# Kernel tuning notes

Hardware: AMD Instinct MI355X
Metric: run time of the kernel (lower is better)

## Reference

```python
import jax, jax.numpy as jnp
import numpy as np

B, I, H = 512, 2048, 2048


def setup_inputs() -> dict:
    key = jax.random.key(0)
    ks = jax.random.split(key, 14)
    s = 0.02  # weight init scale
    inp = {
        "inputs": jax.random.normal(ks[0], (B, I), jnp.float32),
        "states": jax.random.normal(ks[1], (2, B, H), jnp.float32),
        "Wi": jax.random.normal(ks[2], (I, H), jnp.float32) * s,
        "Ui": jax.random.normal(ks[3], (H, H), jnp.float32) * s,
        "bi": jnp.zeros((H,), jnp.float32),
        "Wf": jax.random.normal(ks[4], (I, H), jnp.float32) * s,
        "Uf": jax.random.normal(ks[5], (H, H), jnp.float32) * s,
        "bf": jnp.zeros((H,), jnp.float32),
        "Wg": jax.random.normal(ks[6], (I, H), jnp.float32) * s,
        "Ug": jax.random.normal(ks[7], (H, H), jnp.float32) * s,
        "bg": jnp.zeros((H,), jnp.float32),
        "Wc": jax.random.normal(ks[8], (I, H), jnp.float32) * s,
        "Uc": jax.random.normal(ks[9], (H, H), jnp.float32) * s,
        "bc": jnp.zeros((H,), jnp.float32),
    }
    return inp


def reference(inputs, states, Wi, Ui, bi, Wf, Uf, bf, Wg, Ug, bg, Wc, Uc, bc):
    # Faithful to the original cell, including its quirks:
    # recurrent matmuls use states[0] (prevstate); c mixes states[1] (prevoutput).
    prevstate, prevoutput = states[0], states[1]  # [B,H] each
    i = jax.nn.sigmoid(inputs @ Wi + prevstate @ Ui + bi)
    f = jax.nn.sigmoid(inputs @ Wf + prevstate @ Uf + bf)
    g = jax.nn.sigmoid(inputs @ Wg + prevstate @ Ug + bg)
    c_ = jnp.tanh(inputs @ Wc + prevstate @ Uc + bc)
    c = f * prevoutput + i * c_
    state = g * jnp.tanh(c)
    return c, jnp.stack([state, c])
```

## Files before the change

### kernel.cpp

```cpp
#include <hip/hip_runtime.h>

#define BH (512*2048)
#define PPLANE (512ull*8192ull)
#define PLANE_BYTES (PPLANE*2ull)

typedef __attribute__((ext_vector_type(8))) short short8;
typedef __attribute__((ext_vector_type(4))) float floatx4;
typedef __attribute__((ext_vector_type(4))) unsigned int uint4v;
typedef __attribute__((ext_vector_type(8))) unsigned short ushort8v;

__device__ inline unsigned pk2(float a, float b){
    unsigned ua = __builtin_bit_cast(unsigned, a) + 0x8000u;
    unsigned ub = __builtin_bit_cast(unsigned, b) + 0x8000u;
    return __builtin_amdgcn_perm(ub, ua, 0x07060302u);
}
__device__ inline unsigned short f2bf1(float x){
    return (unsigned short)((__builtin_bit_cast(unsigned, x) + 0x8000u) >> 16);
}
__device__ inline float bf2f(unsigned short s){
    return __builtin_bit_cast(float, ((unsigned)s) << 16);
}
__device__ inline int swz(int r, int g){ return r*4 + (g ^ ((r>>1)&3)); }

__device__ inline float fsig(float x){ return __builtin_amdgcn_rcpf(1.f + __expf(-x)); }
__device__ inline float ftanh(float x){ return 2.f*fsig(2.f*x) - 1.f; }

__global__ __launch_bounds__(256, 2) void gemm_tile(
    const float* __restrict__ inputs, const float* __restrict__ states,
    const float* __restrict__ Wi, const float* __restrict__ Ui,
    const float* __restrict__ Wf, const float* __restrict__ Uf,
    const float* __restrict__ Wg, const float* __restrict__ Ug,
    const float* __restrict__ Wc, const float* __restrict__ Uc,
    unsigned short* __restrict__ P, int KB)
{
    __shared__ uint4v As[2][512];
    __shared__ uint4v Bs[2][512];

    const int t    = threadIdx.x;
    const int m0   = blockIdx.y * 128;
    const int z    = blockIdx.z;
    const int nblk = blockIdx.x;
    const int gate = nblk >> 4;
    const int c0   = (nblk & 15) * 128;
    const int gk   = z * KB;

    const float* Abase; const float* Bsel; int ko;
    if (gk < 2048) {
        Abase = inputs; ko = gk;
        switch (gate){ case 0: Bsel=Wi; break; case 1: Bsel=Wf; break;
                       case 2: Bsel=Wg; break; default: Bsel=Wc; }
    } else {
        Abase = states; ko = gk - 2048;
        switch (gate){ case 0: Bsel=Ui; break; case 1: Bsel=Uf; break;
                       case 2: Bsel=Ug; break; default: Bsel=Uc; }
    }
    const int NIT = KB >> 5;

    const int lane  = t & 63;
    const int wave  = t >> 6;
    const int wm    = (wave & 1) * 64;
    const int wn    = (wave >> 1) * 64;
    const int row16 = lane & 15;
    const int g4    = lane >> 4;

    const int ar  = t >> 2;
    const int ag  = t & 3;
    const int bn  = t & 127;
    const int bg2 = (t >> 7) * 2;

    const float* Ap = Abase + (size_t)(m0 + ar) * 2048 + ko + ag * 8;
    const float* Bp = Bsel  + (size_t)ko * 2048 + c0 + bn;

    floatx4 acc[4][4];
    #pragma unroll
    for (int i = 0; i < 4; i++)
        #pragma unroll
        for (int j = 0; j < 4; j++)
            acc[i][j] = (floatx4){0.f,0.f,0.f,0.f};

    floatx4 a0,a1,a2,a3;
    float b0[8], b1[8];

    a0 = *(const floatx4*)Ap;            a1 = *(const floatx4*)(Ap + 4);
    a2 = *(const floatx4*)(Ap + 64*2048); a3 = *(const floatx4*)(Ap + 64*2048 + 4);
    #pragma unroll
    for (int j = 0; j < 8; j++) b0[j] = Bp[(size_t)(bg2*8 + j) * 2048];
    #pragma unroll
    for (int j = 0; j < 8; j++) b1[j] = Bp[(size_t)(bg2*8 + 8 + j) * 2048];
    {
        uint4v w;
        w.x=pk2(a0[0],a0[1]); w.y=pk2(a0[2],a0[3]); w.z=pk2(a1[0],a1[1]); w.w=pk2(a1[2],a1[3]);
        As[0][swz(ar, ag)] = w;
        w.x=pk2(a2[0],a2[1]); w.y=pk2(a2[2],a2[3]); w.z=pk2(a3[0],a3[1]); w.w=pk2(a3[2],a3[3]);
        As[0][swz(ar+64, ag)] = w;
        w.x=pk2(b0[0],b0[1]); w.y=pk2(b0[2],b0[3]); w.z=pk2(b0[4],b0[5]); w.w=pk2(b0[6],b0[7]);
        Bs[0][swz(bn, bg2)] = w;
        w.x=pk2(b1[0],b1[1]); w.y=pk2(b1[2],b1[3]); w.z=pk2(b1[4],b1[5]); w.w=pk2(b1[6],b1[7]);
        Bs[0][swz(bn, bg2+1)] = w;
    }

    for (int kk = 0; kk < NIT; kk++) {
        __syncthreads();
        const int cur = kk & 1;

        if (kk + 1 < NIT) {
            const float* ap = Ap + (kk+1) * 32;
            a0 = *(const floatx4*)ap;             a1 = *(const floatx4*)(ap + 4);
            a2 = *(const floatx4*)(ap + 64*2048); a3 = *(const floatx4*)(ap + 64*2048 + 4);
            const float* bp = Bp + (size_t)(kk+1) * 32 * 2048;
            #pragma unroll
            for (int j = 0; j < 8; j++) b0[j] = bp[(size_t)(bg2*8 + j) * 2048];
            #pragma unroll
            for (int j = 0; j < 8; j++) b1[j] = bp[(size_t)(bg2*8 + 8 + j) * 2048];
        }

        short8 afr[4], bfr[4];
        #pragma unroll
        for (int mi = 0; mi < 4; mi++)
            afr[mi] = *(const short8*)&As[cur][swz(wm + mi*16 + row16, g4)];
        #pragma unroll
        for (int ni = 0; ni < 4; ni++)
            bfr[ni] = *(const short8*)&Bs[cur][swz(wn + ni*16 + row16, g4)];
        #pragma unroll
        for (int mi = 0; mi < 4; mi++)
            #pragma unroll
            for (int ni = 0; ni < 4; ni++)
                acc[mi][ni] = __builtin_amdgcn_mfma_f32_16x16x32_bf16(
                    afr[mi], bfr[ni], acc[mi][ni], 0, 0, 0);

        if (kk + 1 < NIT) {
            const int nxt = cur ^ 1;
            uint4v w;
            w.x=pk2(a0[0],a0[1]); w.y=pk2(a0[2],a0[3]); w.z=pk2(a1[0],a1[1]); w.w=pk2(a1[2],a1[3]);
            As[nxt][swz(ar, ag)] = w;
            w.x=pk2(a2[0],a2[1]); w.y=pk2(a2[2],a2[3]); w.z=pk2(a3[0],a3[1]); w.w=pk2(a3[2],a3[3]);
            As[nxt][swz(ar+64, ag)] = w;
            w.x=pk2(b0[0],b0[1]); w.y=pk2(b0[2],b0[3]); w.z=pk2(b0[4],b0[5]); w.w=pk2(b0[6],b0[7]);
            Bs[nxt][swz(bn, bg2)] = w;
            w.x=pk2(b1[0],b1[1]); w.y=pk2(b1[2],b1[3]); w.z=pk2(b1[4],b1[5]); w.w=pk2(b1[6],b1[7]);
            Bs[nxt][swz(bn, bg2+1)] = w;
        }
    }

    unsigned short* dst = P + (size_t)z * PPLANE;
    const int gbase = gate * 2048 + c0;
    #pragma unroll
    for (int mi = 0; mi < 4; mi++)
        #pragma unroll
        for (int ni = 0; ni < 4; ni++)
            #pragma unroll
            for (int j = 0; j < 4; j++) {
                int row = m0 + wm + mi*16 + g4*4 + j;
                int col = gbase + wn + ni*16 + row16;
                dst[(size_t)row * 8192 + col] = f2bf1(acc[mi][ni][j]);
            }
}

__global__ __launch_bounds__(256) void combine_kernel(
    float* __restrict__ out, const unsigned short* __restrict__ P,
    const float* __restrict__ states,
    const float* __restrict__ bi, const float* __restrict__ bfv,
    const float* __restrict__ bg, const float* __restrict__ bc, int nz)
{
    const int idx = (blockIdx.x * 256 + threadIdx.x) * 8;
    const int row = idx >> 11;
    const int h   = idx & 2047;
    const size_t base = (size_t)row * 8192 + h;

    float xi[8], xf[8], xg[8], xc[8];
    #pragma unroll
    for (int e = 0; e < 8; e++) {
        xi[e] = bi[h+e]; xf[e] = bfv[h+e]; xg[e] = bg[h+e]; xc[e] = bc[h+e];
    }
    for (int z = 0; z < nz; z++) {
        const unsigned short* Pz = P + (size_t)z * PPLANE;
        ushort8v vi = *(const ushort8v*)&Pz[base];
        ushort8v vf = *(const ushort8v*)&Pz[base + 2048];
        ushort8v vg = *(const ushort8v*)&Pz[base + 4096];
        ushort8v vc = *(const ushort8v*)&Pz[base + 6144];
        #pragma unroll
        for (int e = 0; e < 8; e++) {
            xi[e] += bf2f(vi[e]); xf[e] += bf2f(vf[e]);
            xg[e] += bf2f(vg[e]); xc[e] += bf2f(vc[e]);
        }
    }

    const float* po = states + BH;
    floatx4 pov[2];
    pov[0] = *(const floatx4*)&po[idx];
    pov[1] = *(const floatx4*)&po[idx + 4];

    floatx4 vcv[2], vsv[2];
    #pragma unroll
    for (int q = 0; q < 2; q++)
        #pragma unroll
        for (int j = 0; j < 4; j++) {
            int e = q*4 + j;
            float c = fsig(xf[e]) * pov[q][j] + fsig(xi[e]) * ftanh(xc[e]);
            vcv[q][j] = c;
            vsv[q][j] = fsig(xg[e]) * ftanh(c);
        }
    #pragma unroll
    for (int q = 0; q < 2; q++) {
        *(floatx4*)&out[idx + q*4]          = vcv[q];
        *(floatx4*)&out[BH + idx + q*4]     = vsv[q];
        *(floatx4*)&out[2*BH + idx + q*4]   = vcv[q];
    }
}

extern "C" void kernel_launch(void* const* d_in, const int* in_sizes, int n_in,
                              void* d_out, int out_size, void* d_ws, size_t ws_size,
                              hipStream_t stream) {
    const float* inputs = (const float*)d_in[0];
    const float* states = (const float*)d_in[1];
    const float* Wi = (const float*)d_in[2];
    const float* Ui = (const float*)d_in[3];
    const float* bi = (const float*)d_in[4];
    const float* Wf = (const float*)d_in[5];
    const float* Uf = (const float*)d_in[6];
    const float* bf = (const float*)d_in[7];
    const float* Wg = (const float*)d_in[8];
    const float* Ug = (const float*)d_in[9];
    const float* bg = (const float*)d_in[10];
    const float* Wc = (const float*)d_in[11];
    const float* Uc = (const float*)d_in[12];
    const float* bc = (const float*)d_in[13];
    float* out = (float*)d_out;
    unsigned short* P = (unsigned short*)d_ws;

    const int nz = (ws_size >= 4 * PLANE_BYTES) ? 4 : 2;
    const int KB = 4096 / nz;

    dim3 grid(64, 4, nz);
    gemm_tile<<<grid, 256, 0, stream>>>(inputs, states, Wi, Ui, Wf, Uf,
                                        Wg, Ug, Wc, Uc, P, KB);
    combine_kernel<<<BH / (8 * 256), 256, 0, stream>>>(out, P, states,
                                                       bi, bf, bg, bc, nz);
}
```

Measured before the change: 238.1 us.

## Deepen global-load prefetch to two stages with ping-pong register sets

Restructures the GEMM main loop to keep two register sets (X/Y) of global loads in flight, issuing loads two K-steps ahead instead of one, and unrolls the loop by two. This aims to hide global memory latency for the fp32 A/B tiles better before they are converted to bf16 and stored to LDS. It roughly doubles the registers held for staged loads, which may lower occupancy or cause spills. It also assumes NIT is even, and LOADY(1) is issued unconditionally before the loop.

```diff
diff --git a/kernel.cpp b/kernel.cpp
--- a/kernel.cpp
+++ b/kernel.cpp
@@ -68,8 +68,8 @@
     const int bn  = t & 127;
     const int bg2 = (t >> 7) * 2;
 
-    const float* Ap = Abase + (size_t)(m0 + ar) * 2048 + ko + ag * 8;
-    const float* Bp = Bsel  + (size_t)ko * 2048 + c0 + bn;
+    const float* Ap  = Abase + (size_t)(m0 + ar) * 2048 + ko + ag * 8;
+    const float* Bpt = Bsel  + ((size_t)ko + bg2 * 8) * 2048 + c0 + bn;
 
     floatx4 acc[4][4];
     #pragma unroll
@@ -78,68 +78,81 @@
         for (int j = 0; j < 4; j++)
             acc[i][j] = (floatx4){0.f,0.f,0.f,0.f};
 
-    floatx4 a0,a1,a2,a3;
-    float b0[8], b1[8];
-
-    a0 = *(const floatx4*)Ap;            a1 = *(const floatx4*)(Ap + 4);
-    a2 = *(const floatx4*)(Ap + 64*2048); a3 = *(const floatx4*)(Ap + 64*2048 + 4);
-    #pragma unroll
-    for (int j = 0; j < 8; j++) b0[j] = Bp[(size_t)(bg2*8 + j) * 2048];
-    #pragma unroll
-    for (int j = 0; j < 8; j++) b1[j] = Bp[(size_t)(bg2*8 + 8 + j) * 2048];
-    {
+    floatx4 xa0,xa1,xa2,xa3; float xb0[8], xb1[8];
+    floatx4 ya0,ya1,ya2,ya3; float yb0[8], yb1[8];
+
+    auto LOADX = [&](int k){
+        const float* ap = Ap + k * 32;
+        xa0 = *(const floatx4*)ap;             xa1 = *(const floatx4*)(ap + 4);
+        xa2 = *(const floatx4*)(ap + 64*2048); xa3 = *(const floatx4*)(ap + 64*2048 + 4);
+        const float* bp = Bpt + (size_t)k * 32 * 2048;
+        #pragma unroll
+        for (int j = 0; j < 8; j++) xb0[j] = bp[(size_t)j * 2048];
+        #pragma unroll
+        for (int j = 0; j < 8; j++) xb1[j] = bp[(size_t)(8 + j) * 2048];
+    };
+    auto LOADY = [&](int k){
+        const float* ap = Ap + k * 32;
+        ya0 = *(const floatx4*)ap;             ya1 = *(const floatx4*)(ap + 4);
+        ya2 = *(const floatx4*)(ap + 64*2048); ya3 = *(const floatx4*)(ap + 64*2048 + 4);
+        const float* bp = Bpt + (size_t)k * 32 * 2048;
+        #pragma unroll
+        for (int j = 0; j < 8; j++) yb0[j] = bp[(size_t)j * 2048];
+        #pragma unroll
+        for (int j = 0; j < 8; j++) yb1[j] = bp[(size_t)(8 + j) * 2048];
+    };
+    auto CVTX = [&](int buf){
         uint4v w;
-        w.x=pk2(a0[0],a0[1]); w.y=pk2(a0[2],a0[3]); w.z=pk2(a1[0],a1[1]); w.w=pk2(a1[2],a1[3]);
-        As[0][swz(ar, ag)] = w;
-        w.x=pk2(a2[0],a2[1]); w.y=pk2(a2[2],a2[3]); w.z=pk2(a3[0],a3[1]); w.w=pk2(a3[2],a3[3]);
-        As[0][swz(ar+64, ag)] = w;
-        w.x=pk2(b0[0],b0[1]); w.y=pk2(b0[2],b0[3]); w.z=pk2(b0[4],b0[5]); w.w=pk2(b0[6],b0[7]);
-        Bs[0][swz(bn, bg2)] = w;
-        w.x=pk2(b1[0],b1[1]); w.y=pk2(b1[2],b1[3]); w.z=pk2(b1[4],b1[5]); w.w=pk2(b1[6],b1[7]);
-        Bs[0][swz(bn, bg2+1)] = w;
-    }
-
-    for (int kk = 0; kk < NIT; kk++) {
-        __syncthreads();
-        const int cur = kk & 1;
-
-        if (kk + 1 < NIT) {
-            const float* ap = Ap + (kk+1) * 32;
-            a0 = *(const floatx4*)ap;             a1 = *(const floatx4*)(ap + 4);
-            a2 = *(const floatx4*)(ap + 64*2048); a3 = *(const floatx4*)(ap + 64*2048 + 4);
-            const float* bp = Bp + (size_t)(kk+1) * 32 * 2048;
-            #pragma unroll
-            for (int j = 0; j < 8; j++) b0[j] = bp[(size_t)(bg2*8 + j) * 2048];
-            #pragma unroll
-            for (int j = 0; j < 8; j++) b1[j] = bp[(size_t)(bg2*8 + 8 + j) * 2048];
-        }
-
+        w.x=pk2(xa0[0],xa0[1]); w.y=pk2(xa0[2],xa0[3]); w.z=pk2(xa1[0],xa1[1]); w.w=pk2(xa1[2],xa1[3]);
+        As[buf][swz(ar, ag)] = w;
+        w.x=pk2(xa2[0],xa2[1]); w.y=pk2(xa2[2],xa2[3]); w.z=pk2(xa3[0],xa3[1]); w.w=pk2(xa3[2],xa3[3]);
+        As[buf][swz(ar+64, ag)] = w;
+        w.x=pk2(xb0[0],xb0[1]); w.y=pk2(xb0[2],xb0[3]); w.z=pk2(xb0[4],xb0[5]); w.w=pk2(xb0[6],xb0[7]);
+        Bs[buf][swz(bn, bg2)] = w;
+        w.x=pk2(xb1[0],xb1[1]); w.y=pk2(xb1[2],xb1[3]); w.z=pk2(xb1[4],xb1[5]); w.w=pk2(xb1[6],xb1[7]);
+        Bs[buf][swz(bn, bg2+1)] = w;
+    };
+    auto CVTY = [&](int buf){
+        uint4v w;
+        w.x=pk2(ya0[0],ya0[1]); w.y=pk2(ya0[2],ya0[3]); w.z=pk2(ya1[0],ya1[1]); w.w=pk2(ya1[2],ya1[3]);
+        As[buf][swz(ar, ag)] = w;
+        w.x=pk2(ya2[0],ya2[1]); w.y=pk2(ya2[2],ya2[3]); w.z=pk2(ya3[0],ya3[1]); w.w=pk2(ya3[2],ya3[3]);
+        As[buf][swz(ar+64, ag)] = w;
+        w.x=pk2(yb0[0],yb0[1]); w.y=pk2(yb0[2],yb0[3]); w.z=pk2(yb0[4],yb0[5]); w.w=pk2(yb0[6],yb0[7]);
+        Bs[buf][swz(bn, bg2)] = w;
+        w.x=pk2(yb1[0],yb1[1]); w.y=pk2(yb1[2],yb1[3]); w.z=pk2(yb1[4],yb1[5]); w.w=pk2(yb1[6],yb1[7]);
+        Bs[buf][swz(bn, bg2+1)] = w;
+    };
+    auto MFMAS = [&](int buf){
         short8 afr[4], bfr[4];
         #pragma unroll
         for (int mi = 0; mi < 4; mi++)
-            afr[mi] = *(const short8*)&As[cur][swz(wm + mi*16 + row16, g4)];
+            afr[mi] = *(const short8*)&As[buf][swz(wm + mi*16 + row16, g4)];
         #pragma unroll
         for (int ni = 0; ni < 4; ni++)
-            bfr[ni] = *(const short8*)&Bs[cur][swz(wn + ni*16 + row16, g4)];
+            bfr[ni] = *(const short8*)&Bs[buf][swz(wn + ni*16 + row16, g4)];
         #pragma unroll
         for (int mi = 0; mi < 4; mi++)
             #pragma unroll
             for (int ni = 0; ni < 4; ni++)
                 acc[mi][ni] = __builtin_amdgcn_mfma_f32_16x16x32_bf16(
                     afr[mi], bfr[ni], acc[mi][ni], 0, 0, 0);
-
-        if (kk + 1 < NIT) {
-            const int nxt = cur ^ 1;
-            uint4v w;
-            w.x=pk2(a0[0],a0[1]); w.y=pk2(a0[2],a0[3]); w.z=pk2(a1[0],a1[1]); w.w=pk2(a1[2],a1[3]);
-            As[nxt][swz(ar, ag)] = w;
-            w.x=pk2(a2[0],a2[1]); w.y=pk2(a2[2],a2[3]); w.z=pk2(a3[0],a3[1]); w.w=pk2(a3[2],a3[3]);
-            As[nxt][swz(ar+64, ag)] = w;
-            w.x=pk2(b0[0],b0[1]); w.y=pk2(b0[2],b0[3]); w.z=pk2(b0[4],b0[5]); w.w=pk2(b0[6],b0[7]);
-            Bs[nxt][swz(bn, bg2)] = w;
-            w.x=pk2(b1[0],b1[1]); w.y=pk2(b1[2],b1[3]); w.z=pk2(b1[4],b1[5]); w.w=pk2(b1[6],b1[7]);
-            Bs[nxt][swz(bn, bg2+1)] = w;
-        }
+    };
+
+    LOADX(0);
+    CVTX(0);
+    LOADY(1);
+
+    for (int kk = 0; kk < NIT; kk += 2) {
+        __syncthreads();
+        if (kk + 2 < NIT) LOADX(kk + 2);
+        MFMAS(0);
+        CVTY(1);
+
+        __syncthreads();
+        if (kk + 3 < NIT) LOADY(kk + 3);
+        MFMAS(1);
+        if (kk + 2 < NIT) CVTX(0);
     }
 
     unsigned short* dst = P + (size_t)z * PPLANE;
```

New measurement: 240.4 us. No clear change (+0.9%).

## Pre-convert operands to bf16 tiles and stream them via global_load_lds

Applied to the files above, without the earlier changes.

Adds a prep kernel that converts every weight matrix to bf16 in a tile-major layout and converts inputs and states to bf16. A new GEMM kernel then loads these tiles straight into LDS with global_load_lds, removing the in-loop fp32 loads, bf16 packing and strided column loads of B. The cost is an extra pass that reads all fp32 weights and writes bf16 copies on every call, plus a larger workspace requirement. The old path is kept as a fallback when the workspace is too small.

```diff
diff --git a/kernel.cpp b/kernel.cpp
--- a/kernel.cpp
+++ b/kernel.cpp
@@ -1,14 +1,22 @@
 #include <hip/hip_runtime.h>
 
 #define BH (512*2048)
+#define BHA 1048576ull
 #define PPLANE (512ull*8192ull)
 #define PLANE_BYTES (PPLANE*2ull)
+#define WT_ELEMS (8ull*2048*2048)
+#define AB_ELEMS (2ull*512*2048)
+#define LDT 40
 
 typedef __attribute__((ext_vector_type(8))) short short8;
 typedef __attribute__((ext_vector_type(4))) float floatx4;
 typedef __attribute__((ext_vector_type(4))) unsigned int uint4v;
 typedef __attribute__((ext_vector_type(8))) unsigned short ushort8v;
 
+#define GLOAD_LDS16(g, l) __builtin_amdgcn_global_load_lds( \
+    (const __attribute__((address_space(1))) unsigned int*)(g), \
+    (__attribute__((address_space(3))) unsigned int*)(l), 16, 0, 0)
+
 __device__ inline unsigned pk2(float a, float b){
     unsigned ua = __builtin_bit_cast(unsigned, a) + 0x8000u;
     unsigned ub = __builtin_bit_cast(unsigned, b) + 0x8000u;
@@ -21,9 +29,129 @@
     return __builtin_bit_cast(float, ((unsigned)s) << 16);
 }
 __device__ inline int swz(int r, int g){ return r*4 + (g ^ ((r>>1)&3)); }
-
 __device__ inline float fsig(float x){ return __builtin_amdgcn_rcpf(1.f + __expf(-x)); }
 __device__ inline float ftanh(float x){ return 2.f*fsig(2.f*x) - 1.f; }
+
+__global__ __launch_bounds__(256) void prep(
+    const float* __restrict__ inputs, const float* __restrict__ states,
+    const float* __restrict__ Wi, const float* __restrict__ Ui,
+    const float* __restrict__ Wf, const float* __restrict__ Uf,
+    const float* __restrict__ Wg, const float* __restrict__ Ug,
+    const float* __restrict__ Wc, const float* __restrict__ Uc,
+    unsigned short* __restrict__ Wt, unsigned short* __restrict__ Ab)
+{
+    const int bid = blockIdx.x, tid = threadIdx.x;
+    if (bid < 8192) {
+        const int gate = bid >> 11, r = bid & 2047, nb = r >> 7, kt = r & 127;
+        const float* src; int krow;
+        if (kt < 64) {
+            krow = kt * 32;
+            switch (gate){ case 0: src=Wi; break; case 1: src=Wf; break;
+                           case 2: src=Wg; break; default: src=Wc; }
+        } else {
+            krow = (kt - 64) * 32;
+            switch (gate){ case 0: src=Ui; break; case 1: src=Uf; break;
+                           case 2: src=Ug; break; default: src=Uc; }
+        }
+        const int n_loc = tid >> 1, k_loc = (tid & 1) * 16;
+        const float* sp = src + (size_t)(krow + k_loc) * 2048 + nb * 128 + n_loc;
+        unsigned o[8];
+        #pragma unroll
+        for (int j = 0; j < 8; j++) {
+            float f0 = sp[(size_t)(2*j)   * 2048];
+            float f1 = sp[(size_t)(2*j+1) * 2048];
+            o[j] = pk2(f0, f1);
+        }
+        unsigned short* op = Wt + (size_t)bid * 4096 + n_loc * 32 + k_loc;
+        *(uint4v*)op       = (uint4v){o[0],o[1],o[2],o[3]};
+        *(uint4v*)(op + 8) = (uint4v){o[4],o[5],o[6],o[7]};
+    } else {
+        const size_t off = ((size_t)(bid - 8192) * 256 + tid) * 8;
+        const float* src = (off < BHA) ? (inputs + off) : (states + (off - BHA));
+        floatx4 v0 = *(const floatx4*)src;
+        floatx4 v1 = *(const floatx4*)(src + 4);
+        uint4v w;
+        w.x = pk2(v0[0],v0[1]); w.y = pk2(v0[2],v0[3]);
+        w.z = pk2(v1[0],v1[1]); w.w = pk2(v1[2],v1[3]);
+        *(uint4v*)(Ab + off) = w;
+    }
+}
+
+__global__ __launch_bounds__(256, 4) void gemm_lds(
+    const unsigned short* __restrict__ Wt, const unsigned short* __restrict__ Ab,
+    unsigned short* __restrict__ P)
+{
+    __shared__ unsigned short As[2][4096];
+    __shared__ unsigned short Bs[2][4096];
+
+    const int t = threadIdx.x, lane = t & 63, wave = t >> 6;
+    const int nblk = blockIdx.x, gate = nblk >> 4, nb = nblk & 15;
+    const int m0 = blockIdx.y * 128, z = blockIdx.z;
+
+    const unsigned short* Bt = Wt + ((size_t)(gate*16 + nb) * 128 + z*32) * 4096;
+    const unsigned short* Abase = Ab + (size_t)(z >> 1) * BHA
+                                     + (size_t)m0 * 2048 + (z & 1) * 1024;
+
+    const int i0 = wave * 2, i1 = wave * 2 + 1;
+    const unsigned short* ag0 = Abase + (size_t)(i0*16 + (lane>>2)) * 2048 + (lane&3)*8;
+    const unsigned short* ag1 = Abase + (size_t)(i1*16 + (lane>>2)) * 2048 + (lane&3)*8;
+    const unsigned short* bg0 = Bt + i0*512 + lane*8;
+    const unsigned short* bg1 = Bt + i1*512 + lane*8;
+
+    floatx4 acc[4][4];
+    #pragma unroll
+    for (int i = 0; i < 4; i++)
+        #pragma unroll
+        for (int j = 0; j < 4; j++)
+            acc[i][j] = (floatx4){0.f,0.f,0.f,0.f};
+
+    const int wm = (wave & 1) * 64, wn = (wave >> 1) * 64;
+    const int row16 = lane & 15, g4 = lane >> 4;
+
+    GLOAD_LDS16(ag0, &As[0][i0*512]);
+    GLOAD_LDS16(ag1, &As[0][i1*512]);
+    GLOAD_LDS16(bg0, &Bs[0][i0*512]);
+    GLOAD_LDS16(bg1, &Bs[0][i1*512]);
+    __syncthreads();
+
+    for (int kk = 0; kk < 32; kk++) {
+        const int cur = kk & 1;
+        if (kk < 31) {
+            const int nxt = cur ^ 1;
+            GLOAD_LDS16(ag0 + (kk+1)*32,   &As[nxt][i0*512]);
+            GLOAD_LDS16(ag1 + (kk+1)*32,   &As[nxt][i1*512]);
+            GLOAD_LDS16(bg0 + (kk+1)*4096, &Bs[nxt][i0*512]);
+            GLOAD_LDS16(bg1 + (kk+1)*4096, &Bs[nxt][i1*512]);
+        }
+        short8 afr[4], bfr[4];
+        #pragma unroll
+        for (int mi = 0; mi < 4; mi++)
+            afr[mi] = *(const short8*)&As[cur][(wm + mi*16 + row16)*32 + g4*8];
+        #pragma unroll
+        for (int ni = 0; ni < 4; ni++)
+            bfr[ni] = *(const short8*)&Bs[cur][(wn + ni*16 + row16)*32 + g4*8];
+        #pragma unroll
+        for (int mi = 0; mi < 4; mi++)
+            #pragma unroll
+            for (int ni = 0; ni < 4; ni++)
+                acc[mi][ni] = __builtin_amdgcn_mfma_f32_16x16x32_bf16(
+                    afr[mi], bfr[ni], acc[mi][ni], 0, 0, 0);
+        __syncthreads();
+    }
+
+    unsigned short* dst = P + (size_t)z * PPLANE;
+    const int gbase = gate * 2048 + nb * 128;
+    #pragma unroll
+    for (int mi = 0; mi < 4; mi++)
+        #pragma unroll
+        for (int ni = 0; ni < 4; ni++)
+            #pragma unroll
+            for (int j = 0; j < 4; j++) {
+                int row = m0 + wm + mi*16 + g4*4 + j;
+                int col = gbase + wn + ni*16 + row16;
+                dst[(size_t)row * 8192 + col] = f2bf1(acc[mi][ni][j]);
+            }
+}
 
 __global__ __launch_bounds__(256, 2) void gemm_tile(
     const float* __restrict__ inputs, const float* __restrict__ states,
@@ -36,13 +164,13 @@
     __shared__ uint4v As[2][512];
     __shared__ uint4v Bs[2][512];
 
-    const int t    = threadIdx.x;
-    const int m0   = blockIdx.y * 128;
-    const int z    = blockIdx.z;
+    const int t = threadIdx.x;
+    const int m0 = blockIdx.y * 128;
+    const int z = blockIdx.z;
     const int nblk = blockIdx.x;
     const int gate = nblk >> 4;
-    const int c0   = (nblk & 15) * 128;
-    const int gk   = z * KB;
+    const int c0 = (nblk & 15) * 128;
+    const int gk = z * KB;
 
     const float* Abase; const float* Bsel; int ko;
     if (gk < 2048) {
@@ -56,20 +184,14 @@
     }
     const int NIT = KB >> 5;
 
-    const int lane  = t & 63;
-    const int wave  = t >> 6;
-    const int wm    = (wave & 1) * 64;
-    const int wn    = (wave >> 1) * 64;
-    const int row16 = lane & 15;
-    const int g4    = lane >> 4;
-
-    const int ar  = t >> 2;
-    const int ag  = t & 3;
-    const int bn  = t & 127;
-    const int bg2 = (t >> 7) * 2;
+    const int lane = t & 63, wave = t >> 6;
+    const int wm = (wave & 1) * 64, wn = (wave >> 1) * 64;
+    const int row16 = lane & 15, g4 = lane >> 4;
+    const int ar = t >> 2, ag = t & 3;
+    const int bn = t & 127, bg2 = (t >> 7) * 2;
 
     const float* Ap = Abase + (size_t)(m0 + ar) * 2048 + ko + ag * 8;
-    const float* Bp = Bsel  + (size_t)ko * 2048 + c0 + bn;
+    const float* Bp = Bsel + (size_t)ko * 2048 + c0 + bn;
 
     floatx4 acc[4][4];
     #pragma unroll
@@ -78,10 +200,8 @@
         for (int j = 0; j < 4; j++)
             acc[i][j] = (floatx4){0.f,0.f,0.f,0.f};
 
-    floatx4 a0,a1,a2,a3;
-    float b0[8], b1[8];
-
-    a0 = *(const floatx4*)Ap;            a1 = *(const floatx4*)(Ap + 4);
+    floatx4 a0,a1,a2,a3; float b0[8], b1[8];
+    a0 = *(const floatx4*)Ap;             a1 = *(const floatx4*)(Ap + 4);
     a2 = *(const floatx4*)(Ap + 64*2048); a3 = *(const floatx4*)(Ap + 64*2048 + 4);
     #pragma unroll
     for (int j = 0; j < 8; j++) b0[j] = Bp[(size_t)(bg2*8 + j) * 2048];
@@ -102,7 +222,6 @@
     for (int kk = 0; kk < NIT; kk++) {
         __syncthreads();
         const int cur = kk & 1;
-
         if (kk + 1 < NIT) {
             const float* ap = Ap + (kk+1) * 32;
             a0 = *(const floatx4*)ap;             a1 = *(const floatx4*)(ap + 4);
@@ -113,7 +232,6 @@
             #pragma unroll
             for (int j = 0; j < 8; j++) b1[j] = bp[(size_t)(bg2*8 + 8 + j) * 2048];
         }
-
         short8 afr[4], bfr[4];
         #pragma unroll
         for (int mi = 0; mi < 4; mi++)
@@ -127,7 +245,6 @@
             for (int ni = 0; ni < 4; ni++)
                 acc[mi][ni] = __builtin_amdgcn_mfma_f32_16x16x32_bf16(
                     afr[mi], bfr[ni], acc[mi][ni], 0, 0, 0);
-
         if (kk + 1 < NIT) {
             const int nxt = cur ^ 1;
             uint4v w;
@@ -164,7 +281,7 @@
 {
     const int idx = (blockIdx.x * 256 + threadIdx.x) * 8;
     const int row = idx >> 11;
-    const int h   = idx & 2047;
+    const int h = idx & 2047;
     const size_t base = (size_t)row * 8192 + h;
 
     float xi[8], xf[8], xg[8], xc[8];
@@ -202,9 +319,9 @@
         }
     #pragma unroll
     for (int q = 0; q < 2; q++) {
-        *(floatx4*)&out[idx + q*4]          = vcv[q];
-        *(floatx4*)&out[BH + idx + q*4]     = vsv[q];
-        *(floatx4*)&out[2*BH + idx + q*4]   = vcv[q];
+        *(floatx4*)&out[idx + q*4]        = vcv[q];
+        *(floatx4*)&out[BH + idx + q*4]   = vsv[q];
+        *(floatx4*)&out[2*BH + idx + q*4] = vcv[q];
     }
 }
 
@@ -226,14 +343,25 @@
     const float* Uc = (const float*)d_in[12];
     const float* bc = (const float*)d_in[13];
     float* out = (float*)d_out;
-    unsigned short* P = (unsigned short*)d_ws;
-
-    const int nz = (ws_size >= 4 * PLANE_BYTES) ? 4 : 2;
-    const int KB = 4096 / nz;
-
-    dim3 grid(64, 4, nz);
-    gemm_tile<<<grid, 256, 0, stream>>>(inputs, states, Wi, Ui, Wf, Uf,
-                                        Wg, Ug, Wc, Uc, P, KB);
-    combine_kernel<<<BH / (8 * 256), 256, 0, stream>>>(out, P, states,
-                                                       bi, bf, bg, bc, nz);
-}
+
+    const size_t need = (WT_ELEMS + AB_ELEMS + 4 * PPLANE) * 2;
+    if (ws_size >= need) {
+        unsigned short* Wt = (unsigned short*)d_ws;
+        unsigned short* Ab = Wt + WT_ELEMS;
+        unsigned short* P  = Ab + AB_ELEMS;
+        prep<<<9216, 256, 0, stream>>>(inputs, states, Wi, Ui, Wf, Uf,
+                                       Wg, Ug, Wc, Uc, Wt, Ab);
+        gemm_lds<<<dim3(64, 4, 4), 256, 0, stream>>>(Wt, Ab, P);
+        combine_kernel<<<BH / (8 * 256), 256, 0, stream>>>(out, P, states,
+                                                           bi, bf, bg, bc, 4);
+    } else {
+        unsigned short* P = (unsigned short*)d_ws;
+        const int nz = (ws_size >= 4 * PLANE_BYTES) ? 4 : 2;
+        const int KB = 4096 / nz;
+        dim3 grid(64, 4, nz);
+        gemm_tile<<<grid, 256, 0, stream>>>(inputs, states, Wi, Ui, Wf, Uf,
+                                            Wg, Ug, Wc, Uc, P, KB);
+        combine_kernel<<<BH / (8 * 256), 256, 0, stream>>>(out, P, states,
+                                                           bi, bf, bg, bc, nz);
+    }
+}
```

Measured after the change: 232.0 us. 1.03x faster.
